# Optimization experiments

Hardware: AMD Instinct MI355X
Metric: run time of the kernel (lower is better)

The kernel has to match this reference:

```python
import jax, jax.numpy as jnp
import numpy as np

H = 16        # num query heads
HKV = 4       # num kv heads
D = 128       # head_dim
HID = 2048    # hidden_size
G = H // HKV  # heads per kv group


def setup_inputs() -> dict:
    key = jax.random.key(0)
    ks = jax.random.split(key, 9)
    s = 0.02
    x = jax.random.normal(ks[0], (2, 2048, HID), dtype=jnp.float32)
    wq = jax.random.normal(ks[1], (HID, H * D), dtype=jnp.float32) * s
    bq = jnp.zeros((H * D,), jnp.float32)
    wk = jax.random.normal(ks[2], (HID, HKV * D), dtype=jnp.float32) * s
    bk = jnp.zeros((HKV * D,), jnp.float32)
    wv = jax.random.normal(ks[3], (HID, HKV * D), dtype=jnp.float32) * s
    bv = jnp.zeros((HKV * D,), jnp.float32)
    wo = jax.random.normal(ks[4], (HID, HID), dtype=jnp.float32) * s
    bo = jnp.zeros((HID,), jnp.float32)
    return dict(x=x, wq=wq, bq=bq, wk=wk, bk=bk, wv=wv, bv=bv, wo=wo, bo=bo)


def reference(x, wq, bq, wk, bk, wv, bv, wo, bo):
    B, S, _ = x.shape
    scale = jnp.float32(1.0 / np.sqrt(D))
    # projections (torch Linear with weight stored as [in, out] here)
    q = (x @ wq + bq).reshape(B, S, H, D)          # [B,S,H,D]
    k = (x @ wk + bk).reshape(B, S, HKV, D)        # [B,S,Hkv,D]
    v = (x @ wv + bv).reshape(B, S, HKV, D)
    # group query heads by kv head instead of expanding KV
    q = q.reshape(B, S, HKV, G, D)
    scores = jnp.einsum('bqhgd,bkhd->bhgqk', q, k) * scale  # [B,Hkv,G,S,S]
    causal = jnp.triu(jnp.ones((S, S), dtype=bool), k=1)
    scores = jnp.where(causal, jnp.float32(-1e9), scores)
    weights = jax.nn.softmax(scores, axis=-1)
    out = jnp.einsum('bhgqk,bkhd->bqhgd', weights, v)        # [B,S,Hkv,G,D]
    out = out.reshape(B, S, H * D)
    return out @ wo + bo
```

## Files before the change

### kernel.cpp

```cpp
#include <hip/hip_runtime.h>
#include <hip/hip_bf16.h>
#include <math.h>

#define HID 2048
#define NH 16
#define NKV 4
#define HD 128
#define GQ 4
#define BATCH 2

typedef short short8v __attribute__((ext_vector_type(8)));
typedef float f32x4 __attribute__((ext_vector_type(4)));

__device__ __forceinline__ ushort f2bf(float f) {
  uint u = __float_as_uint(f);
  uint r = (u + 0x7fffu + ((u >> 16) & 1u)) >> 16;
  return (ushort)r;
}

__device__ __forceinline__ void gld_lds16(const void* g, void* lds) {
  __builtin_amdgcn_global_load_lds(
      (const __attribute__((address_space(1))) unsigned int*)g,
      (__attribute__((address_space(3))) unsigned int*)lds, 16, 0, 0);
}

#define WAVE_LDS_FENCE()                                \
  do {                                                  \
    asm volatile("s_waitcnt lgkmcnt(0)" ::: "memory");  \
    __builtin_amdgcn_sched_barrier(0);                  \
  } while (0)

__global__ __launch_bounds__(256) void castx_kernel(
    const float* __restrict__ x, ushort* __restrict__ xb) {
  const int i = ((int)blockIdx.x * 256 + (int)threadIdx.x) * 8;
  float4 f0 = *reinterpret_cast<const float4*>(x + i);
  float4 f1 = *reinterpret_cast<const float4*>(x + i + 4);
  uint4 o;
  o.x = (uint)f2bf(f0.x) | ((uint)f2bf(f0.y) << 16);
  o.y = (uint)f2bf(f0.z) | ((uint)f2bf(f0.w) << 16);
  o.z = (uint)f2bf(f1.x) | ((uint)f2bf(f1.y) << 16);
  o.w = (uint)f2bf(f1.z) | ((uint)f2bf(f1.w) << 16);
  *reinterpret_cast<uint4*>(xb + i) = o;
}

__global__ __launch_bounds__(256) void tcast_kernel(
    const float* __restrict__ W, ushort* __restrict__ Wt, int K, int N) {
  __shared__ float T[32][33];
  const int k0 = blockIdx.x * 32;
  const int n0 = blockIdx.y * 32;
  const int t = threadIdx.x;
  const int r = t >> 3;
  const int c4 = (t & 7) * 4;
  float4 vin = *reinterpret_cast<const float4*>(
      &W[(size_t)(k0 + r) * N + n0 + c4]);
  T[c4 + 0][r] = vin.x;
  T[c4 + 1][r] = vin.y;
  T[c4 + 2][r] = vin.z;
  T[c4 + 3][r] = vin.w;
  __syncthreads();
  ushort4 o;
  o.x = f2bf(T[r][c4 + 0]);
  o.y = f2bf(T[r][c4 + 1]);
  o.z = f2bf(T[r][c4 + 2]);
  o.w = f2bf(T[r][c4 + 3]);
  *reinterpret_cast<ushort4*>(&Wt[(size_t)(n0 + r) * K + k0 + c4]) = o;
}

template <int MODE>
__global__ __launch_bounds__(256) void gemm_big(
    const ushort* __restrict__ A,
    const ushort* __restrict__ W0, const ushort* __restrict__ W1,
    const ushort* __restrict__ W2,
    const float* __restrict__ b0, const float* __restrict__ b1,
    const float* __restrict__ b2,
    void* __restrict__ C0, void* __restrict__ C1, void* __restrict__ C2,
    int M, int K, int S) {
  __shared__ ushort As[2][128 * 32];
  __shared__ ushort Bs[2][128 * 32];
  const int tid = threadIdx.x;
  const int m0 = blockIdx.y * 128;
  const int n0 = blockIdx.x * 128;
  const int wave = tid >> 6;
  const int lane = tid & 63;
  const int quad = lane >> 4;
  const int lr = lane & 15;
  const int l4 = lane >> 2;
  const int lc = (lane & 3) * 8;
  const int wm = (wave >> 1) * 64;
  const int wn = (wave & 1) * 64;

  const ushort* Wt;
  const float* bias;
  int nloc, Nout, om;
  void* Cout;
  if (MODE == 0) {
    Wt = W0; bias = b0; nloc = n0; Nout = 2048; om = 0; Cout = C0;
  } else {
    if (n0 < 2048)      { Wt = W0; bias = b0; nloc = n0;        Nout = 2048; om = 1; Cout = C0; }
    else if (n0 < 2560) { Wt = W1; bias = b1; nloc = n0 - 2048; Nout = 512;  om = 1; Cout = C1; }
    else                { Wt = W2; bias = b2; nloc = n0 - 2560; Nout = 512;  om = 2; Cout = C2; }
  }

  f32x4 acc[4][4];
#pragma unroll
  for (int i = 0; i < 4; ++i)
#pragma unroll
    for (int j = 0; j < 4; ++j) acc[i][j] = (f32x4){0.f, 0.f, 0.f, 0.f};

  const size_t rowA = (size_t)(m0 + wave * 32 + l4) * K + lc;
  const size_t rowB = (size_t)(nloc + wave * 32 + l4) * K + lc;

#define STAGE_GEMM(t, bi)                                                  \
  do {                                                                     \
    const int kof = (t) * 32;                                              \
    gld_lds16(&A[rowA + kof], &As[bi][(wave * 32) * 32]);                  \
    gld_lds16(&A[rowA + 16 * K + kof], &As[bi][(wave * 32 + 16) * 32]);    \
    gld_lds16(&Wt[rowB + kof], &Bs[bi][(wave * 32) * 32]);                 \
    gld_lds16(&Wt[rowB + 16 * K + kof], &Bs[bi][(wave * 32 + 16) * 32]);   \
  } while (0)

  const int nt = K / 32;
  STAGE_GEMM(0, 0);

  for (int t = 0; t < nt; ++t) {
    const int cur = t & 1;
    __builtin_amdgcn_s_barrier();
    if (t + 1 < nt) {
      STAGE_GEMM(t + 1, cur ^ 1);
      asm volatile("s_waitcnt vmcnt(4)" ::: "memory");
    } else {
      asm volatile("s_waitcnt vmcnt(0)" ::: "memory");
    }
    __builtin_amdgcn_s_barrier();
    __builtin_amdgcn_sched_barrier(0);

    short8v af[4], bf[4];
#pragma unroll
    for (int x = 0; x < 4; ++x) {
      const int ra = wm + x * 16 + lr;
      af[x] = *reinterpret_cast<const short8v*>(&As[cur][ra * 32 + quad * 8]);
      const int rb = wn + x * 16 + lr;
      bf[x] = *reinterpret_cast<const short8v*>(&Bs[cur][rb * 32 + quad * 8]);
    }
#pragma unroll
    for (int i = 0; i < 4; ++i)
#pragma unroll
      for (int j = 0; j < 4; ++j)
        acc[i][j] = __builtin_amdgcn_mfma_f32_16x16x32_bf16(
            af[i], bf[j], acc[i][j], 0, 0, 0);
  }
#undef STAGE_GEMM

#pragma unroll
  for (int i = 0; i < 4; ++i) {
    const int row_base = m0 + wm + i * 16 + quad * 4;
#pragma unroll
    for (int j = 0; j < 4; ++j) {
      const int col = nloc + wn + j * 16 + lr;
      const float b = bias[col];
      if (om == 0) {
        float* C = (float*)Cout;
#pragma unroll
        for (int rg = 0; rg < 4; ++rg)
          C[(size_t)(row_base + rg) * Nout + col] = acc[i][j][rg] + b;
      } else if (om == 1) {
        ushort* C = (ushort*)Cout;
#pragma unroll
        for (int rg = 0; rg < 4; ++rg)
          C[(size_t)(row_base + rg) * Nout + col] = f2bf(acc[i][j][rg] + b);
      } else {
        ushort* C = (ushort*)Cout;
        const int bb = (row_base >= S) ? 1 : 0;
        const int s = row_base - bb * S;
        const int kvh = col >> 7;
        const int d = col & 127;
        ushort4 o;
        o.x = f2bf(acc[i][j][0] + b);
        o.y = f2bf(acc[i][j][1] + b);
        o.z = f2bf(acc[i][j][2] + b);
        o.w = f2bf(acc[i][j][3] + b);
        *reinterpret_cast<ushort4*>(
            &C[((size_t)(bb * NKV + kvh) * HD + d) * S + s]) = o;
      }
    }
  }
}

__device__ __forceinline__ void stage_kv_dma(
    const ushort* __restrict__ Kb, const ushort* __restrict__ Vb,
    ushort* Kdst, ushort* Vdst, int k0, int S, int wave, int lane) {
  const int rK = lane >> 4, cK = lane & 15;
  const int rV = lane >> 3, cV = lane & 7;
#pragma unroll
  for (int c = 0; c < 4; ++c) {
    const int g = wave * 4 + c;
    const int row = g * 4 + rK;
    const int jk = cK ^ (row & 15);
    gld_lds16(&Kb[(size_t)(k0 + row) * (NKV * HD) + jk * 8], &Kdst[g * 512]);
    const int d = g * 8 + rV;
    const int jv = cV ^ (d & 7);
    gld_lds16(&Vb[(size_t)d * S + k0 + jv * 8], &Vdst[g * 512]);
  }
}

__global__ __launch_bounds__(256, 2) void gqa_attn_mfma(
    const ushort* __restrict__ Qg, const ushort* __restrict__ Kgl,
    const ushort* __restrict__ Vt_g, ushort* __restrict__ O, int S) {
  __shared__ ushort Ks0[64 * 128];
  __shared__ ushort Ks1[64 * 128];
  __shared__ ushort Vs0[128 * 64];
  __shared__ ushort Vs1[128 * 64];
  __shared__ ushort Ps[4][16][72];

  const int tid = threadIdx.x;
  const int wave = tid >> 6;
  const int lane = tid & 63;
  const int quad = lane >> 4;
  const int lr = lane & 15;
  const int q0 = ((int)gridDim.x - 1 - (int)blockIdx.x) * 64;
  const int hq = blockIdx.y;
  const int b = blockIdx.z;
  const int kvh = hq >> 2;
  const float scale = 0.08838834764831845f;

  const ushort* Qb = Qg + ((size_t)b * S) * (NH * HD) + (size_t)hq * HD;
  const ushort* Kb = Kgl + ((size_t)b * S) * (NKV * HD) + (size_t)kvh * HD;
  const ushort* Vb = Vt_g + ((size_t)(b * NKV + kvh) * HD) * S;

#pragma unroll
  for (int i = 0; i < 4; ++i) {
    const int id = tid + i * 256;
    const int r = id >> 4, c = id & 15;
    const int p = c ^ (r & 15);
    *reinterpret_cast<uint4*>(&Ks1[r * 128 + p * 8]) =
        *reinterpret_cast<const uint4*>(
            &Qb[(size_t)(q0 + r) * (NH * HD) + c * 8]);
  }
  __syncthreads();
  short8v aq[4];
  {
    const int ra = wave * 16 + lr;
#pragma unroll
    for (int ks = 0; ks < 4; ++ks)
      aq[ks] = *reinterpret_cast<const short8v*>(
          &Ks1[ra * 128 + (((ks * 4 + quad) ^ lr) & 15) * 8]);
  }
  WAVE_LDS_FENCE();

  f32x4 oacc[8];
#pragma unroll
  for (int nb = 0; nb < 8; ++nb) oacc[nb] = (f32x4){0.f, 0.f, 0.f, 0.f};
  float l_r = 0.f;

  const int ntiles = q0 / 64 + 1;

  stage_kv_dma(Kb, Vb, Ks0, Vs0, 0, S, wave, lane);

  for (int kt = 0; kt < ntiles; ++kt) {
    const int k0 = kt * 64;
    const ushort* Kc = (kt & 1) ? Ks1 : Ks0;
    const ushort* Vc = (kt & 1) ? Vs1 : Vs0;

    __builtin_amdgcn_s_barrier();
    if (kt + 1 < ntiles) {
      ushort* Kn = (kt & 1) ? Ks0 : Ks1;
      ushort* Vn = (kt & 1) ? Vs0 : Vs1;
      stage_kv_dma(Kb, Vb, Kn, Vn, k0 + 64, S, wave, lane);
      asm volatile("s_waitcnt vmcnt(8)" ::: "memory");
    } else {
      asm volatile("s_waitcnt vmcnt(0)" ::: "memory");
    }
    __builtin_amdgcn_s_barrier();
    __builtin_amdgcn_sched_barrier(0);

    f32x4 sacc[4];
    __builtin_amdgcn_s_setprio(1);
#pragma unroll
    for (int nb = 0; nb < 4; ++nb) {
      sacc[nb] = (f32x4){0.f, 0.f, 0.f, 0.f};
      const int rb = nb * 16 + lr;
#pragma unroll
      for (int ks = 0; ks < 4; ++ks) {
        short8v bk = *reinterpret_cast<const short8v*>(
            &Kc[rb * 128 + (((ks * 4 + quad) ^ lr) & 15) * 8]);
        sacc[nb] = __builtin_amdgcn_mfma_f32_16x16x32_bf16(
            bk, aq[ks], sacc[nb], 0, 0, 0);
      }
    }
    __builtin_amdgcn_s_setprio(0);

    const bool diag = (kt == ntiles - 1);
    const int qi = q0 + wave * 16 + lr;
    float pv[4][4];
    float rs = 0.f;
#pragma unroll
    for (int nb = 0; nb < 4; ++nb) {
#pragma unroll
      for (int rg = 0; rg < 4; ++rg) {
        float sv = sacc[nb][rg] * scale;
        if (diag) {
          const int kj = k0 + nb * 16 + quad * 4 + rg;
          if (kj > qi) sv = -1e30f;
        }
        const float p = __expf(sv);
        pv[nb][rg] = p;
        rs += p;
      }
    }
    rs += __shfl_xor(rs, 16);
    rs += __shfl_xor(rs, 32);
    l_r += rs;

#pragma unroll
    for (int nb = 0; nb < 4; ++nb) {
      ushort4 o;
      o.x = f2bf(pv[nb][0]);
      o.y = f2bf(pv[nb][1]);
      o.z = f2bf(pv[nb][2]);
      o.w = f2bf(pv[nb][3]);
      *reinterpret_cast<ushort4*>(&Ps[wave][lr][nb * 16 + quad * 4]) = o;
    }

    WAVE_LDS_FENCE();

    short8v ap[2];
#pragma unroll
    for (int ks = 0; ks < 2; ++ks)
      ap[ks] = *reinterpret_cast<const short8v*>(
          &Ps[wave][lr][ks * 32 + quad * 8]);
    __builtin_amdgcn_s_setprio(1);
#pragma unroll
    for (int nb = 0; nb < 8; ++nb) {
      const int rv = nb * 16 + lr;
#pragma unroll
      for (int ks = 0; ks < 2; ++ks) {
        short8v bv = *reinterpret_cast<const short8v*>(
            &Vc[rv * 64 + (((ks * 4 + quad) ^ lr) & 7) * 8]);
        oacc[nb] = __builtin_amdgcn_mfma_f32_16x16x32_bf16(
            ap[ks], bv, oacc[nb], 0, 0, 0);
      }
    }
    __builtin_amdgcn_s_setprio(0);
  }

  const float invl = 1.0f / l_r;
  float inv[4];
#pragma unroll
  for (int rg = 0; rg < 4; ++rg)
    inv[rg] = __shfl(invl, (lane & 48) | (quad * 4 + rg));
  __syncthreads();
  ushort* ow = &Ks0[wave * 16 * 128];
#pragma unroll
  for (int nb = 0; nb < 8; ++nb)
#pragma unroll
    for (int rg = 0; rg < 4; ++rg)
      ow[(quad * 4 + rg) * 128 + nb * 16 + lr] = f2bf(oacc[nb][rg] * inv[rg]);
  WAVE_LDS_FENCE();
  ushort* Ob = O + ((size_t)b * S) * (NH * HD) + (size_t)hq * HD;
#pragma unroll
  for (int ii = 0; ii < 4; ++ii) {
    const int id = lane + ii * 64;
    const int r16 = id >> 4, c = id & 15;
    uint4 val = *reinterpret_cast<const uint4*>(&ow[r16 * 128 + c * 8]);
    *reinterpret_cast<uint4*>(
        &Ob[(size_t)(q0 + wave * 16 + r16) * (NH * HD) + c * 8]) = val;
  }
}

extern "C" void kernel_launch(void* const* d_in, const int* in_sizes, int n_in,
                              void* d_out, int out_size, void* d_ws,
                              size_t ws_size, hipStream_t stream) {
  const float* x = (const float*)d_in[0];
  const float* wq = (const float*)d_in[1];
  const float* bq = (const float*)d_in[2];
  const float* wk = (const float*)d_in[3];
  const float* bk = (const float*)d_in[4];
  const float* wv = (const float*)d_in[5];
  const float* bv = (const float*)d_in[6];
  const float* wo = (const float*)d_in[7];
  const float* bo = (const float*)d_in[8];
  float* out = (float*)d_out;

  const int M = in_sizes[0] / HID;
  const int S = M / BATCH;

  char* w = (char*)d_ws;
  ushort* xb    = (ushort*)(w + 0);
  ushort* qb    = (ushort*)(w + (16u << 20));
  ushort* kb    = (ushort*)(w + (32u << 20));
  ushort* vT    = (ushort*)(w + (36u << 20));
  ushort* attnb = (ushort*)(w + (40u << 20));
  ushort* wqT   = (ushort*)(w + (56u << 20));
  ushort* wkT   = (ushort*)(w + (64u << 20));
  ushort* wvT   = (ushort*)(w + (66u << 20));
  ushort* woT   = (ushort*)(w + (68u << 20));

  dim3 blk(256);
  castx_kernel<<<dim3((M * HID) / (8 * 256)), blk, 0, stream>>>(x, xb);
  tcast_kernel<<<dim3(HID / 32, (NH * HD) / 32), blk, 0, stream>>>(
      wq, wqT, HID, NH * HD);
  tcast_kernel<<<dim3(HID / 32, (NKV * HD) / 32), blk, 0, stream>>>(
      wk, wkT, HID, NKV * HD);
  tcast_kernel<<<dim3(HID / 32, (NKV * HD) / 32), blk, 0, stream>>>(
      wv, wvT, HID, NKV * HD);
  tcast_kernel<<<dim3(HID / 32, HID / 32), blk, 0, stream>>>(
      wo, woT, HID, HID);

  gemm_big<1><<<dim3(3072 / 128, M / 128), blk, 0, stream>>>(
      xb, wqT, wkT, wvT, bq, bk, bv, qb, kb, vT, M, HID, S);

  gqa_attn_mfma<<<dim3(S / 64, NH, BATCH), blk, 0, stream>>>(
      qb, kb, vT, attnb, S);

  gemm_big<0><<<dim3(HID / 128, M / 128), blk, 0, stream>>>(
      attnb, woT, nullptr, nullptr, bo, nullptr, nullptr,
      out, nullptr, nullptr, M, HID, S);
}
```

Before: 348.6 us.

## Use 128-query, 8-wave attention blocks and pass P through shuffles instead of LDS

The attention kernel now processes 128 query rows per block with 512 threads (8 waves), so each staged K/V tile is shared by twice as many waves and each block does half as much staging per query. The causal tile count and masking are adjusted so the last two key tiles are masked. The softmax probabilities are packed into registers and rearranged into MFMA A-operand layout with cross-lane shuffles, which removes the per-wave LDS P buffer and its fence. In exchange there are more shuffle instructions, more masking work on the final tiles, and fewer, larger blocks, which may leave the GPU less evenly loaded.

```diff
diff --git a/kernel.cpp b/kernel.cpp
--- a/kernel.cpp
+++ b/kernel.cpp
@@ -186,14 +186,14 @@
   }
 }
 
-__device__ __forceinline__ void stage_kv_dma(
+__device__ __forceinline__ void stage_kv_dma8(
     const ushort* __restrict__ Kb, const ushort* __restrict__ Vb,
     ushort* Kdst, ushort* Vdst, int k0, int S, int wave, int lane) {
   const int rK = lane >> 4, cK = lane & 15;
   const int rV = lane >> 3, cV = lane & 7;
 #pragma unroll
-  for (int c = 0; c < 4; ++c) {
-    const int g = wave * 4 + c;
+  for (int c = 0; c < 2; ++c) {
+    const int g = wave * 2 + c;
     const int row = g * 4 + rK;
     const int jk = cK ^ (row & 15);
     gld_lds16(&Kb[(size_t)(k0 + row) * (NKV * HD) + jk * 8], &Kdst[g * 512]);
@@ -203,21 +203,21 @@
   }
 }
 
-__global__ __launch_bounds__(256, 2) void gqa_attn_mfma(
+__global__ __launch_bounds__(512, 4) void gqa_attn_mfma(
     const ushort* __restrict__ Qg, const ushort* __restrict__ Kgl,
     const ushort* __restrict__ Vt_g, ushort* __restrict__ O, int S) {
-  __shared__ ushort Ks0[64 * 128];
-  __shared__ ushort Ks1[64 * 128];
-  __shared__ ushort Vs0[128 * 64];
-  __shared__ ushort Vs1[128 * 64];
-  __shared__ ushort Ps[4][16][72];
+  __shared__ __align__(16) ushort L[32768];
+  ushort* K0 = L;
+  ushort* K1 = L + 8192;
+  ushort* V0 = L + 16384;
+  ushort* V1 = L + 24576;
 
   const int tid = threadIdx.x;
   const int wave = tid >> 6;
   const int lane = tid & 63;
   const int quad = lane >> 4;
   const int lr = lane & 15;
-  const int q0 = ((int)gridDim.x - 1 - (int)blockIdx.x) * 64;
+  const int q0 = ((int)gridDim.x - 1 - (int)blockIdx.x) * 128;
   const int hq = blockIdx.y;
   const int b = blockIdx.z;
   const int kvh = hq >> 2;
@@ -229,10 +229,10 @@
 
 #pragma unroll
   for (int i = 0; i < 4; ++i) {
-    const int id = tid + i * 256;
+    const int id = tid + i * 512;
     const int r = id >> 4, c = id & 15;
     const int p = c ^ (r & 15);
-    *reinterpret_cast<uint4*>(&Ks1[r * 128 + p * 8]) =
+    *reinterpret_cast<uint4*>(&L[r * 128 + p * 8]) =
         *reinterpret_cast<const uint4*>(
             &Qb[(size_t)(q0 + r) * (NH * HD) + c * 8]);
   }
@@ -243,30 +243,34 @@
 #pragma unroll
     for (int ks = 0; ks < 4; ++ks)
       aq[ks] = *reinterpret_cast<const short8v*>(
-          &Ks1[ra * 128 + (((ks * 4 + quad) ^ lr) & 15) * 8]);
-  }
-  WAVE_LDS_FENCE();
+          &L[ra * 128 + (((ks * 4 + quad) ^ lr) & 15) * 8]);
+  }
+  __syncthreads();
 
   f32x4 oacc[8];
 #pragma unroll
   for (int nb = 0; nb < 8; ++nb) oacc[nb] = (f32x4){0.f, 0.f, 0.f, 0.f};
   float l_r = 0.f;
 
-  const int ntiles = q0 / 64 + 1;
-
-  stage_kv_dma(Kb, Vb, Ks0, Vs0, 0, S, wave, lane);
+  const int ntiles = q0 / 64 + 2;
+
+  const int laneA = ((quad * 2) & 3) * 16 + lr;
+  const int laneB = ((quad * 2 + 1) & 3) * 16 + lr;
+  const bool hi = (quad >= 2);
+
+  stage_kv_dma8(Kb, Vb, K0, V0, 0, S, wave, lane);
 
   for (int kt = 0; kt < ntiles; ++kt) {
     const int k0 = kt * 64;
-    const ushort* Kc = (kt & 1) ? Ks1 : Ks0;
-    const ushort* Vc = (kt & 1) ? Vs1 : Vs0;
+    const ushort* Kc = (kt & 1) ? K1 : K0;
+    const ushort* Vc = (kt & 1) ? V1 : V0;
 
     __builtin_amdgcn_s_barrier();
     if (kt + 1 < ntiles) {
-      ushort* Kn = (kt & 1) ? Ks0 : Ks1;
-      ushort* Vn = (kt & 1) ? Vs0 : Vs1;
-      stage_kv_dma(Kb, Vb, Kn, Vn, k0 + 64, S, wave, lane);
-      asm volatile("s_waitcnt vmcnt(8)" ::: "memory");
+      ushort* Kn = (kt & 1) ? K0 : K1;
+      ushort* Vn = (kt & 1) ? V0 : V1;
+      stage_kv_dma8(Kb, Vb, Kn, Vn, k0 + 64, S, wave, lane);
+      asm volatile("s_waitcnt vmcnt(4)" ::: "memory");
     } else {
       asm volatile("s_waitcnt vmcnt(0)" ::: "memory");
     }
@@ -289,45 +293,49 @@
     }
     __builtin_amdgcn_s_setprio(0);
 
-    const bool diag = (kt == ntiles - 1);
+    const bool needmask = (kt + 2 >= ntiles);
     const int qi = q0 + wave * 16 + lr;
-    float pv[4][4];
+    uint u[4][2];
     float rs = 0.f;
 #pragma unroll
     for (int nb = 0; nb < 4; ++nb) {
+      float p[4];
 #pragma unroll
       for (int rg = 0; rg < 4; ++rg) {
         float sv = sacc[nb][rg] * scale;
-        if (diag) {
+        if (needmask) {
           const int kj = k0 + nb * 16 + quad * 4 + rg;
           if (kj > qi) sv = -1e30f;
         }
-        const float p = __expf(sv);
-        pv[nb][rg] = p;
-        rs += p;
+        p[rg] = __expf(sv);
+        rs += p[rg];
       }
+      u[nb][0] = (uint)f2bf(p[0]) | ((uint)f2bf(p[1]) << 16);
+      u[nb][1] = (uint)f2bf(p[2]) | ((uint)f2bf(p[3]) << 16);
     }
     rs += __shfl_xor(rs, 16);
     rs += __shfl_xor(rs, 32);
     l_r += rs;
 
-#pragma unroll
-    for (int nb = 0; nb < 4; ++nb) {
-      ushort4 o;
-      o.x = f2bf(pv[nb][0]);
-      o.y = f2bf(pv[nb][1]);
-      o.z = f2bf(pv[nb][2]);
-      o.w = f2bf(pv[nb][3]);
-      *reinterpret_cast<ushort4*>(&Ps[wave][lr][nb * 16 + quad * 4]) = o;
-    }
-
-    WAVE_LDS_FENCE();
-
     short8v ap[2];
 #pragma unroll
-    for (int ks = 0; ks < 2; ++ks)
-      ap[ks] = *reinterpret_cast<const short8v*>(
-          &Ps[wave][lr][ks * 32 + quad * 8]);
+    for (int ks = 0; ks < 2; ++ks) {
+      const uint w0a = __shfl(u[2 * ks + 0][0], laneA);
+      const uint w0b = __shfl(u[2 * ks + 1][0], laneA);
+      const uint w1a = __shfl(u[2 * ks + 0][1], laneA);
+      const uint w1b = __shfl(u[2 * ks + 1][1], laneA);
+      const uint w2a = __shfl(u[2 * ks + 0][0], laneB);
+      const uint w2b = __shfl(u[2 * ks + 1][0], laneB);
+      const uint w3a = __shfl(u[2 * ks + 0][1], laneB);
+      const uint w3b = __shfl(u[2 * ks + 1][1], laneB);
+      uint4 q4;
+      q4.x = hi ? w0b : w0a;
+      q4.y = hi ? w1b : w1a;
+      q4.z = hi ? w2b : w2a;
+      q4.w = hi ? w3b : w3a;
+      ap[ks] = *reinterpret_cast<short8v*>(&q4);
+    }
+
     __builtin_amdgcn_s_setprio(1);
 #pragma unroll
     for (int nb = 0; nb < 8; ++nb) {
@@ -349,7 +357,7 @@
   for (int rg = 0; rg < 4; ++rg)
     inv[rg] = __shfl(invl, (lane & 48) | (quad * 4 + rg));
   __syncthreads();
-  ushort* ow = &Ks0[wave * 16 * 128];
+  ushort* ow = &L[wave * 16 * 128];
 #pragma unroll
   for (int nb = 0; nb < 8; ++nb)
 #pragma unroll
@@ -409,7 +417,7 @@
   gemm_big<1><<<dim3(3072 / 128, M / 128), blk, 0, stream>>>(
       xb, wqT, wkT, wvT, bq, bk, bv, qb, kb, vT, M, HID, S);
 
-  gqa_attn_mfma<<<dim3(S / 64, NH, BATCH), blk, 0, stream>>>(
+  gqa_attn_mfma<<<dim3(S / 128, NH, BATCH), dim3(512), 0, stream>>>(
       qb, kb, vT, attnb, S);
 
   gemm_big<0><<<dim3(HID / 128, M / 128), blk, 0, stream>>>(
```

Measured after the change: 333.9 us. 1.04x faster.
